# Performance work log

Measured on AMD Instinct MI355X. Metric: run time of the kernel, lower is better.

## Reference

```python
import jax, jax.numpy as jnp
import numpy as np

EPS = 1e-5

def setup_inputs() -> dict:
    key = jax.random.key(0)
    k1, k2 = jax.random.split(key)
    N, D, O = 32768, 4096, 256
    x = jax.random.normal(k1, (N, D), dtype=jnp.float32)
    gamma = jnp.ones((D,), dtype=jnp.float32)
    beta = jnp.zeros((D,), dtype=jnp.float32)
    W = jax.random.normal(k2, (O, D), dtype=jnp.float32) * (1.0 / np.sqrt(D))
    b = jnp.zeros((O,), dtype=jnp.float32)
    return {"x": x, "gamma": gamma, "beta": beta, "W": W, "b": b}


def reference(x, gamma, beta, W, b):
    # BatchNorm1d in training mode: per-feature batch mean and biased variance
    mean = jnp.mean(x, axis=0)                      # [D]
    var = jnp.mean(jnp.square(x - mean), axis=0)    # [D], biased (divide by N)
    xhat = (x - mean) * jax.lax.rsqrt(var + EPS)
    h = jax.nn.relu(xhat * gamma + beta)            # [N, D]
    # Linear projection
    return h @ W.T + b                               # [N, O]
```

## Files before the change

### kernel.cpp

```cpp
#include <hip/hip_runtime.h>
#include <hip/hip_bf16.h>

#define NROWS 32768
#define DDIM  4096
#define ODIM  256
#define EPSV  1e-5f

#define CHUNKS 128
#define RPC    256

#define BM 128
#define BK 64
#define NKT (DDIM / BK)

typedef __attribute__((ext_vector_type(4))) float          f32x4;
typedef __attribute__((ext_vector_type(8))) __bf16         bf16x8;
typedef __attribute__((ext_vector_type(8))) unsigned short u16x8;
typedef __attribute__((ext_vector_type(4))) unsigned short u16x4;

static __device__ __forceinline__ unsigned short f2bf(float f) {
  return __builtin_bit_cast(unsigned short, __float2bfloat16(f));
}

__global__ __launch_bounds__(256) void k1_stats(const float* __restrict__ x,
                                                float* __restrict__ psum,
                                                float* __restrict__ psq) {
  const int col = blockIdx.x * 1024 + threadIdx.x * 4;
  const float* p = x + (size_t)blockIdx.y * RPC * DDIM + col;
  f32x4 s = {0.f, 0.f, 0.f, 0.f};
  f32x4 q = {0.f, 0.f, 0.f, 0.f};
#pragma unroll 8
  for (int r = 0; r < RPC; ++r) {
    f32x4 v = *(const f32x4*)p;
    p += DDIM;
    s += v;
    q += v * v;
  }
  *(f32x4*)(psum + (size_t)blockIdx.y * DDIM + col) = s;
  *(f32x4*)(psq  + (size_t)blockIdx.y * DDIM + col) = q;
}

__global__ __launch_bounds__(256) void k2_stats_finalize(
    const float* __restrict__ psum, const float* __restrict__ psq,
    const float* __restrict__ gamma, const float* __restrict__ beta,
    float* __restrict__ scale, float* __restrict__ shift) {
  __shared__ float ss[4][64];
  __shared__ float sq[4][64];
  const int lane = threadIdx.x & 63;
  const int g    = threadIdx.x >> 6;
  const int d    = blockIdx.x * 64 + lane;
  float s = 0.f, qq = 0.f;
  for (int c = g * 32; c < (g + 1) * 32; ++c) {
    s  += psum[(size_t)c * DDIM + d];
    qq += psq [(size_t)c * DDIM + d];
  }
  ss[g][lane] = s;
  sq[g][lane] = qq;
  __syncthreads();
  if (g == 0) {
    s  = ss[0][lane] + ss[1][lane] + ss[2][lane] + ss[3][lane];
    qq = sq[0][lane] + sq[1][lane] + sq[2][lane] + sq[3][lane];
    const float inv = 1.0f / (float)NROWS;
    const float mean = s * inv;
    const float var  = fmaxf(qq * inv - mean * mean, 0.f);
    const float a = gamma[d] * rsqrtf(var + EPSV);
    scale[d] = a;
    shift[d] = beta[d] - mean * a;
  }
}

__global__ __launch_bounds__(256) void k2_wconv(const float* __restrict__ Wf,
                                                unsigned short* __restrict__ Wb) {
  const size_t i = ((size_t)blockIdx.x * 256 + threadIdx.x) * 4;
  f32x4 v = *(const f32x4*)(Wf + i);
  u16x4 o;
  o[0] = f2bf(v[0]); o[1] = f2bf(v[1]); o[2] = f2bf(v[2]); o[3] = f2bf(v[3]);
  *(u16x4*)(Wb + i) = o;
}

__global__ __launch_bounds__(512, 1) void k3_bn_gemm(
    const float* __restrict__ x,
    const unsigned short* __restrict__ Wb,
    const float* __restrict__ scale,
    const float* __restrict__ shift,
    const float* __restrict__ bias,
    float* __restrict__ out) {
  __shared__ unsigned short As[2][BM * BK];
  __shared__ unsigned short Bs[2][ODIM * BK];
  __shared__ float SF[DDIM];
  __shared__ float SH[DDIM];

  const int tid = threadIdx.x;
  const int l   = tid & 63;
  const int w   = tid >> 6;
  const int wr  = w >> 2;
  const int wc  = w & 3;
  const size_t bm0 = (size_t)blockIdx.x * BM;

  ((f32x4*)SF)[tid * 2]     = ((const f32x4*)scale)[tid * 2];
  ((f32x4*)SF)[tid * 2 + 1] = ((const f32x4*)scale)[tid * 2 + 1];
  ((f32x4*)SH)[tid * 2]     = ((const f32x4*)shift)[tid * 2];
  ((f32x4*)SH)[tid * 2 + 1] = ((const f32x4*)shift)[tid * 2 + 1];

  const int rA = tid >> 3;
  const int uA = tid & 7;
  const float* xp0 = x + (bm0 + rA) * (size_t)DDIM + uA * 8;
  const float* xp1 = xp0 + (size_t)64 * DDIM;
  const int awo = rA * 64 + ((uA ^ (rA & 7)) << 3);
  int ktb = uA * 8;

  const unsigned short* bsrc[4];
#pragma unroll
  for (int q = 0; q < 4; ++q) {
    const int p  = w * 256 + q * 64 + l;
    const int o  = p >> 3;
    const int up = p & 7;
    bsrc[q] = Wb + (size_t)o * DDIM + ((up ^ (o & 7)) << 3);
  }

  int offA[4], offB[4];
#pragma unroll
  for (int i = 0; i < 4; ++i) {
    const int row = wr * 64 + i * 16 + (l & 15);
    offA[i] = row * 64 + (((l >> 4) ^ (row & 7)) << 3);
  }
#pragma unroll
  for (int j = 0; j < 4; ++j) {
    const int row = wc * 64 + j * 16 + (l & 15);
    offB[j] = row * 64 + (((l >> 4) ^ (row & 7)) << 3);
  }

  const f32x4 zero = {0.f, 0.f, 0.f, 0.f};
  f32x4 acc[4][4];
#pragma unroll
  for (int i = 0; i < 4; ++i)
#pragma unroll
    for (int j = 0; j < 4; ++j) acc[i][j] = zero;

  f32x4 sA0[4], sA1[4];

#define ISSUE_A(S)                                                             \
  asm volatile("global_load_dwordx4 %0, %1, off" : "=v"(S[0]) : "v"(xp0));     \
  asm volatile("global_load_dwordx4 %0, %1, off" : "=v"(S[1]) : "v"(xp0 + 4)); \
  asm volatile("global_load_dwordx4 %0, %1, off" : "=v"(S[2]) : "v"(xp1));     \
  asm volatile("global_load_dwordx4 %0, %1, off" : "=v"(S[3]) : "v"(xp1 + 4)); \
  xp0 += BK; xp1 += BK;                                                        \
  asm volatile("" ::: "memory");

#define ISSUE_B(BUFI)                                                          \
  _Pragma("unroll")                                                            \
  for (int q = 0; q < 4; ++q) {                                                \
    __builtin_amdgcn_global_load_lds(                                          \
        (__attribute__((address_space(1))) void*)bsrc[q],                      \
        (__attribute__((address_space(3))) void*)(                             \
            &Bs[BUFI][(w * 256 + q * 64) * 8]),                                \
        16, 0, 0);                                                             \
    bsrc[q] += BK;                                                             \
  }                                                                            \
  asm volatile("" ::: "memory");

#define TRANSFORM_WRITE(BUFI, S)                                               \
  {                                                                            \
    f32x4 sa0 = *(const f32x4*)&SF[ktb];                                       \
    f32x4 sa1 = *(const f32x4*)&SF[ktb + 4];                                   \
    f32x4 sc0 = *(const f32x4*)&SH[ktb];                                       \
    f32x4 sc1 = *(const f32x4*)&SH[ktb + 4];                                   \
    ktb += BK;                                                                 \
    u16x8 pk0, pk1;                                                            \
    _Pragma("unroll")                                                          \
    for (int e = 0; e < 4; ++e) {                                              \
      pk0[e]     = f2bf(fmaxf(S[0][e] * sa0[e] + sc0[e], 0.f));                \
      pk0[e + 4] = f2bf(fmaxf(S[1][e] * sa1[e] + sc1[e], 0.f));                \
      pk1[e]     = f2bf(fmaxf(S[2][e] * sa0[e] + sc0[e], 0.f));                \
      pk1[e + 4] = f2bf(fmaxf(S[3][e] * sa1[e] + sc1[e], 0.f));                \
    }                                                                          \
    *(u16x8*)&As[BUFI][awo]        = pk0;                                      \
    *(u16x8*)&As[BUFI][awo + 4096] = pk1;                                      \
  }

#define MFMA_PHASE(BUFI)                                                       \
  _Pragma("unroll")                                                            \
  for (int kk = 0; kk < 2; ++kk) {                                             \
    const int kx = kk << 5;                                                    \
    bf16x8 af[4], bfr[4];                                                      \
    _Pragma("unroll")                                                          \
    for (int i = 0; i < 4; ++i)                                                \
      af[i] = __builtin_bit_cast(bf16x8,                                       \
                                 *(const u16x8*)&As[BUFI][offA[i] ^ kx]);      \
    _Pragma("unroll")                                                          \
    for (int j = 0; j < 4; ++j)                                                \
      bfr[j] = __builtin_bit_cast(bf16x8,                                      \
                                  *(const u16x8*)&Bs[BUFI][offB[j] ^ kx]);     \
    _Pragma("unroll")                                                          \
    for (int i = 0; i < 4; ++i)                                                \
      _Pragma("unroll")                                                        \
      for (int j = 0; j < 4; ++j)                                              \
        acc[i][j] = __builtin_amdgcn_mfma_f32_16x16x32_bf16(                   \
            af[i], bfr[j], acc[i][j], 0, 0, 0);                                \
  }

  {
    ISSUE_A(sA0);
    ISSUE_B(0);
    ISSUE_A(sA1);
    asm volatile("s_waitcnt lgkmcnt(0)" ::: "memory");
    __builtin_amdgcn_sched_barrier(0);
    __builtin_amdgcn_s_barrier();
    asm volatile("s_waitcnt vmcnt(8)" ::: "memory");
    __builtin_amdgcn_sched_barrier(0);
    TRANSFORM_WRITE(0, sA0);
    asm volatile("s_waitcnt vmcnt(4) lgkmcnt(0)" ::: "memory");
    __builtin_amdgcn_sched_barrier(0);
    __builtin_amdgcn_s_barrier();
  }

#define STEP_FULL(CUR, SC, SN)                                                 \
  do {                                                                         \
    ISSUE_B((CUR) ^ 1);                                                        \
    ISSUE_A(SC);                                                               \
    MFMA_PHASE(CUR);                                                           \
    asm volatile("s_waitcnt vmcnt(8)" ::: "memory");                           \
    __builtin_amdgcn_sched_barrier(0);                                         \
    TRANSFORM_WRITE((CUR) ^ 1, SN);                                            \
    asm volatile("s_waitcnt vmcnt(4) lgkmcnt(0)" ::: "memory");                \
    __builtin_amdgcn_sched_barrier(0);                                         \
    __builtin_amdgcn_s_barrier();                                              \
  } while (0)

  for (int kt = 0; kt < NKT - 2; kt += 2) {
    STEP_FULL(0, sA0, sA1);
    STEP_FULL(1, sA1, sA0);
  }
  {
    ISSUE_B(1);
    MFMA_PHASE(0);
    asm volatile("s_waitcnt vmcnt(4)" ::: "memory");
    __builtin_amdgcn_sched_barrier(0);
    TRANSFORM_WRITE(1, sA1);
    asm volatile("s_waitcnt vmcnt(0) lgkmcnt(0)" ::: "memory");
    __builtin_amdgcn_sched_barrier(0);
    __builtin_amdgcn_s_barrier();
  }
  MFMA_PHASE(1);

#undef STEP_FULL
#undef MFMA_PHASE
#undef TRANSFORM_WRITE
#undef ISSUE_B
#undef ISSUE_A

  const int cl = l & 15;
  const int rg = l >> 4;
#pragma unroll
  for (int j = 0; j < 4; ++j) {
    const int oc = wc * 64 + j * 16 + cl;
    const float bv = bias[oc];
#pragma unroll
    for (int i = 0; i < 4; ++i) {
      const size_t r0 = bm0 + wr * 64 + i * 16 + rg * 4;
#pragma unroll
      for (int rr = 0; rr < 4; ++rr) {
        out[(r0 + rr) * ODIM + oc] = acc[i][j][rr] + bv;
      }
    }
  }
}

extern "C" void kernel_launch(void* const* d_in, const int* in_sizes, int n_in,
                              void* d_out, int out_size, void* d_ws, size_t ws_size,
                              hipStream_t stream) {
  const float* x     = (const float*)d_in[0];
  const float* gamma = (const float*)d_in[1];
  const float* beta  = (const float*)d_in[2];
  const float* W     = (const float*)d_in[3];
  const float* b     = (const float*)d_in[4];
  float* out = (float*)d_out;

  float* psum  = (float*)d_ws;
  float* psq   = psum + (size_t)CHUNKS * DDIM;
  float* scale = psum + 2 * (size_t)CHUNKS * DDIM;
  float* shift = scale + DDIM;
  unsigned short* Wb = (unsigned short*)(shift + DDIM);

  k1_stats<<<dim3(4, CHUNKS), 256, 0, stream>>>(x, psum, psq);
  k2_stats_finalize<<<DDIM / 64, 256, 0, stream>>>(psum, psq, gamma, beta, scale, shift);
  k2_wconv<<<(ODIM * DDIM) / 1024, 256, 0, stream>>>(W, Wb);
  k3_bn_gemm<<<NROWS / BM, 512, 0, stream>>>(x, Wb, scale, shift, b, out);
}
```

Measured before the change: 246.7 us.

## Warp-specialize BN-GEMM into producer and MFMA consumer waves

Restructures the fused BN+GEMM kernel into 768-thread blocks in which 4 producer waves load x, apply the BN scale/shift/ReLU, convert to bf16 and fill the LDS buffers, while 8 consumer waves only run MFMAs on double-buffered tiles. The aim is to take global-load latency and transform work off the MFMA waves and overlap them through barrier-separated ping-pong stages. In exchange the producers carry twice the load and transform work per thread, and every stage now ends in a full block barrier. The launch bounds change to (768,3), which tightens the register budget.

```diff
diff --git a/kernel.cpp b/kernel.cpp
--- a/kernel.cpp
+++ b/kernel.cpp
@@ -78,7 +78,7 @@
   *(u16x4*)(Wb + i) = o;
 }
 
-__global__ __launch_bounds__(512, 1) void k3_bn_gemm(
+__global__ __launch_bounds__(768, 3) void k3_bn_gemm(
     const float* __restrict__ x,
     const unsigned short* __restrict__ Wb,
     const float* __restrict__ scale,
@@ -92,32 +92,12 @@
 
   const int tid = threadIdx.x;
   const int l   = tid & 63;
-  const int w   = tid >> 6;
-  const int wr  = w >> 2;
-  const int wc  = w & 3;
   const size_t bm0 = (size_t)blockIdx.x * BM;
-
-  ((f32x4*)SF)[tid * 2]     = ((const f32x4*)scale)[tid * 2];
-  ((f32x4*)SF)[tid * 2 + 1] = ((const f32x4*)scale)[tid * 2 + 1];
-  ((f32x4*)SH)[tid * 2]     = ((const f32x4*)shift)[tid * 2];
-  ((f32x4*)SH)[tid * 2 + 1] = ((const f32x4*)shift)[tid * 2 + 1];
-
-  const int rA = tid >> 3;
-  const int uA = tid & 7;
-  const float* xp0 = x + (bm0 + rA) * (size_t)DDIM + uA * 8;
-  const float* xp1 = xp0 + (size_t)64 * DDIM;
-  const int awo = rA * 64 + ((uA ^ (rA & 7)) << 3);
-  int ktb = uA * 8;
-
-  const unsigned short* bsrc[4];
-#pragma unroll
-  for (int q = 0; q < 4; ++q) {
-    const int p  = w * 256 + q * 64 + l;
-    const int o  = p >> 3;
-    const int up = p & 7;
-    bsrc[q] = Wb + (size_t)o * DDIM + ((up ^ (o & 7)) << 3);
-  }
-
+  const bool consumer = (tid < 512);
+
+  const int w  = tid >> 6;
+  const int wr = w >> 2;
+  const int wc = w & 3;
   int offA[4], offB[4];
 #pragma unroll
   for (int i = 0; i < 4; ++i) {
@@ -129,7 +109,6 @@
     const int row = wc * 64 + j * 16 + (l & 15);
     offB[j] = row * 64 + (((l >> 4) ^ (row & 7)) << 3);
   }
-
   const f32x4 zero = {0.f, 0.f, 0.f, 0.f};
   f32x4 acc[4][4];
 #pragma unroll
@@ -137,46 +116,89 @@
 #pragma unroll
     for (int j = 0; j < 4; ++j) acc[i][j] = zero;
 
-  f32x4 sA0[4], sA1[4];
-
-#define ISSUE_A(S)                                                             \
-  asm volatile("global_load_dwordx4 %0, %1, off" : "=v"(S[0]) : "v"(xp0));     \
-  asm volatile("global_load_dwordx4 %0, %1, off" : "=v"(S[1]) : "v"(xp0 + 4)); \
-  asm volatile("global_load_dwordx4 %0, %1, off" : "=v"(S[2]) : "v"(xp1));     \
-  asm volatile("global_load_dwordx4 %0, %1, off" : "=v"(S[3]) : "v"(xp1 + 4)); \
-  xp0 += BK; xp1 += BK;                                                        \
+  const int p  = tid - 512;
+  const int r0 = (p >> 3) & 31;
+  const int uA = p & 7;
+  const float* xr0 = x + (bm0 + r0) * (size_t)DDIM + uA * 8;
+  const float* xr1 = xr0 + (size_t)32 * DDIM;
+  const float* xr2 = xr0 + (size_t)64 * DDIM;
+  const float* xr3 = xr0 + (size_t)96 * DDIM;
+  const int awo = r0 * 64 + ((uA ^ (r0 & 7)) << 3);
+  int ktb = uA * 8;
+  const unsigned short* bsrc[8];
+#pragma unroll
+  for (int q = 0; q < 8; ++q) {
+    const int u  = q * 256 + p;
+    const int o  = u >> 3;
+    const int up = u & 7;
+    bsrc[q] = Wb + (size_t)o * DDIM + ((up ^ (o & 7)) << 3);
+  }
+  const int pwbase = (p & ~63);
+
+  if (!consumer) {
+    const int c0 = p * 16;
+#pragma unroll
+    for (int e = 0; e < 4; ++e) {
+      *(f32x4*)&SF[c0 + e * 4] = *(const f32x4*)(scale + c0 + e * 4);
+      *(f32x4*)&SH[c0 + e * 4] = *(const f32x4*)(shift + c0 + e * 4);
+    }
+  }
+  __syncthreads();
+
+#define ISSUE_A8(S)                                                            \
+  asm volatile("global_load_dwordx4 %0, %1, off"           : "=v"(S[0]) : "v"(xr0)); \
+  asm volatile("global_load_dwordx4 %0, %1, off offset:16" : "=v"(S[1]) : "v"(xr0)); \
+  asm volatile("global_load_dwordx4 %0, %1, off"           : "=v"(S[2]) : "v"(xr1)); \
+  asm volatile("global_load_dwordx4 %0, %1, off offset:16" : "=v"(S[3]) : "v"(xr1)); \
+  asm volatile("global_load_dwordx4 %0, %1, off"           : "=v"(S[4]) : "v"(xr2)); \
+  asm volatile("global_load_dwordx4 %0, %1, off offset:16" : "=v"(S[5]) : "v"(xr2)); \
+  asm volatile("global_load_dwordx4 %0, %1, off"           : "=v"(S[6]) : "v"(xr3)); \
+  asm volatile("global_load_dwordx4 %0, %1, off offset:16" : "=v"(S[7]) : "v"(xr3)); \
+  xr0 += BK; xr1 += BK; xr2 += BK; xr3 += BK;                                  \
   asm volatile("" ::: "memory");
 
-#define ISSUE_B(BUFI)                                                          \
+#define ISSUE_B8(BUFI)                                                         \
   _Pragma("unroll")                                                            \
-  for (int q = 0; q < 4; ++q) {                                                \
+  for (int q = 0; q < 8; ++q) {                                                \
     __builtin_amdgcn_global_load_lds(                                          \
         (__attribute__((address_space(1))) void*)bsrc[q],                      \
         (__attribute__((address_space(3))) void*)(                             \
-            &Bs[BUFI][(w * 256 + q * 64) * 8]),                                \
+            &Bs[BUFI][(q * 256 + pwbase) * 8]),                                \
         16, 0, 0);                                                             \
     bsrc[q] += BK;                                                             \
   }                                                                            \
   asm volatile("" ::: "memory");
 
-#define TRANSFORM_WRITE(BUFI, S)                                               \
+#define TRANSFORM4(BUFI, S)                                                    \
   {                                                                            \
     f32x4 sa0 = *(const f32x4*)&SF[ktb];                                       \
     f32x4 sa1 = *(const f32x4*)&SF[ktb + 4];                                   \
     f32x4 sc0 = *(const f32x4*)&SH[ktb];                                       \
     f32x4 sc1 = *(const f32x4*)&SH[ktb + 4];                                   \
     ktb += BK;                                                                 \
-    u16x8 pk0, pk1;                                                            \
-    _Pragma("unroll")                                                          \
-    for (int e = 0; e < 4; ++e) {                                              \
-      pk0[e]     = f2bf(fmaxf(S[0][e] * sa0[e] + sc0[e], 0.f));                \
-      pk0[e + 4] = f2bf(fmaxf(S[1][e] * sa1[e] + sc1[e], 0.f));                \
-      pk1[e]     = f2bf(fmaxf(S[2][e] * sa0[e] + sc0[e], 0.f));                \
-      pk1[e + 4] = f2bf(fmaxf(S[3][e] * sa1[e] + sc1[e], 0.f));                \
+    _Pragma("unroll")                                                          \
+    for (int k = 0; k < 4; ++k) {                                              \
+      u16x8 pk;                                                                \
+      _Pragma("unroll")                                                        \
+      for (int e = 0; e < 4; ++e) {                                            \
+        pk[e]     = f2bf(fmaxf(S[2 * k][e]     * sa0[e] + sc0[e], 0.f));       \
+        pk[e + 4] = f2bf(fmaxf(S[2 * k + 1][e] * sa1[e] + sc1[e], 0.f));       \
+      }                                                                        \
+      *(u16x8*)&As[BUFI][awo + k * 2048] = pk;                                 \
     }                                                                          \
-    *(u16x8*)&As[BUFI][awo]        = pk0;                                      \
-    *(u16x8*)&As[BUFI][awo + 4096] = pk1;                                      \
-  }
+  }
+
+#define PRODUCE(BUFI)                                                          \
+  do {                                                                         \
+    f32x4 S[8];                                                                \
+    ISSUE_A8(S);                                                               \
+    ISSUE_B8(BUFI);                                                            \
+    asm volatile("s_waitcnt vmcnt(8)" ::: "memory");                           \
+    __builtin_amdgcn_sched_barrier(0);                                         \
+    TRANSFORM4(BUFI, S);                                                       \
+    asm volatile("s_waitcnt vmcnt(0) lgkmcnt(0)" ::: "memory");                \
+    __builtin_amdgcn_sched_barrier(0);                                         \
+  } while (0)
 
 #define MFMA_PHASE(BUFI)                                                       \
   _Pragma("unroll")                                                            \
@@ -199,68 +221,39 @@
             af[i], bfr[j], acc[i][j], 0, 0, 0);                                \
   }
 
-  {
-    ISSUE_A(sA0);
-    ISSUE_B(0);
-    ISSUE_A(sA1);
-    asm volatile("s_waitcnt lgkmcnt(0)" ::: "memory");
-    __builtin_amdgcn_sched_barrier(0);
+  if (!consumer) PRODUCE(0);
+  __builtin_amdgcn_s_barrier();
+
+  for (int kt = 0; kt < NKT - 2; kt += 2) {
+    if (consumer) { MFMA_PHASE(0); } else { PRODUCE(1); }
     __builtin_amdgcn_s_barrier();
-    asm volatile("s_waitcnt vmcnt(8)" ::: "memory");
-    __builtin_amdgcn_sched_barrier(0);
-    TRANSFORM_WRITE(0, sA0);
-    asm volatile("s_waitcnt vmcnt(4) lgkmcnt(0)" ::: "memory");
-    __builtin_amdgcn_sched_barrier(0);
+    if (consumer) { MFMA_PHASE(1); } else { PRODUCE(0); }
     __builtin_amdgcn_s_barrier();
   }
-
-#define STEP_FULL(CUR, SC, SN)                                                 \
-  do {                                                                         \
-    ISSUE_B((CUR) ^ 1);                                                        \
-    ISSUE_A(SC);                                                               \
-    MFMA_PHASE(CUR);                                                           \
-    asm volatile("s_waitcnt vmcnt(8)" ::: "memory");                           \
-    __builtin_amdgcn_sched_barrier(0);                                         \
-    TRANSFORM_WRITE((CUR) ^ 1, SN);                                            \
-    asm volatile("s_waitcnt vmcnt(4) lgkmcnt(0)" ::: "memory");                \
-    __builtin_amdgcn_sched_barrier(0);                                         \
-    __builtin_amdgcn_s_barrier();                                              \
-  } while (0)
-
-  for (int kt = 0; kt < NKT - 2; kt += 2) {
-    STEP_FULL(0, sA0, sA1);
-    STEP_FULL(1, sA1, sA0);
-  }
-  {
-    ISSUE_B(1);
-    MFMA_PHASE(0);
-    asm volatile("s_waitcnt vmcnt(4)" ::: "memory");
-    __builtin_amdgcn_sched_barrier(0);
-    TRANSFORM_WRITE(1, sA1);
-    asm volatile("s_waitcnt vmcnt(0) lgkmcnt(0)" ::: "memory");
-    __builtin_amdgcn_sched_barrier(0);
-    __builtin_amdgcn_s_barrier();
-  }
-  MFMA_PHASE(1);
-
-#undef STEP_FULL
+  if (consumer) { MFMA_PHASE(0); } else { PRODUCE(1); }
+  __builtin_amdgcn_s_barrier();
+  if (consumer) { MFMA_PHASE(1); }
+
 #undef MFMA_PHASE
-#undef TRANSFORM_WRITE
-#undef ISSUE_B
-#undef ISSUE_A
-
-  const int cl = l & 15;
-  const int rg = l >> 4;
-#pragma unroll
-  for (int j = 0; j < 4; ++j) {
-    const int oc = wc * 64 + j * 16 + cl;
-    const float bv = bias[oc];
-#pragma unroll
-    for (int i = 0; i < 4; ++i) {
-      const size_t r0 = bm0 + wr * 64 + i * 16 + rg * 4;
-#pragma unroll
-      for (int rr = 0; rr < 4; ++rr) {
-        out[(r0 + rr) * ODIM + oc] = acc[i][j][rr] + bv;
+#undef PRODUCE
+#undef TRANSFORM4
+#undef ISSUE_B8
+#undef ISSUE_A8
+
+  if (consumer) {
+    const int cl = l & 15;
+    const int rg = l >> 4;
+#pragma unroll
+    for (int j = 0; j < 4; ++j) {
+      const int oc = wc * 64 + j * 16 + cl;
+      const float bv = bias[oc];
+#pragma unroll
+      for (int i = 0; i < 4; ++i) {
+        const size_t rbase = bm0 + wr * 64 + i * 16 + rg * 4;
+#pragma unroll
+        for (int rr = 0; rr < 4; ++rr) {
+          out[(rbase + rr) * ODIM + oc] = acc[i][j][rr] + bv;
+        }
       }
     }
   }
@@ -285,5 +278,5 @@
   k1_stats<<<dim3(4, CHUNKS), 256, 0, stream>>>(x, psum, psq);
   k2_stats_finalize<<<DDIM / 64, 256, 0, stream>>>(psum, psq, gamma, beta, scale, shift);
   k2_wconv<<<(ODIM * DDIM) / 1024, 256, 0, stream>>>(W, Wb);
-  k3_bn_gemm<<<NROWS / BM, 512, 0, stream>>>(x, Wb, scale, shift, b, out);
-}
+  k3_bn_gemm<<<NROWS / BM, 768, 0, stream>>>(x, Wb, scale, shift, b, out);
+}
```

Result: slower. 256.7 us (+4.1%).

## Feed A fragments straight from registers, dropping the LDS A tile

Applied to the files above, without the earlier changes.

Each wave now owns 16 full rows of the 128-row block and loads x directly in the layout the MFMA A operand expects. It normalizes and packs those values to bf16 in registers and passes them into the MFMA without staging through shared memory. Each wave computes all 256 output columns, so it reads 16 B fragments per k-step from LDS instead of 4 A plus 4 B. This removes the LDS writes and reads for A and the associated bank traffic. The cost is four times as many B-fragment LDS reads per wave and less reuse of each B load across rows.

```diff
diff --git a/kernel.cpp b/kernel.cpp
--- a/kernel.cpp
+++ b/kernel.cpp
@@ -85,7 +85,6 @@
     const float* __restrict__ shift,
     const float* __restrict__ bias,
     float* __restrict__ out) {
-  __shared__ unsigned short As[2][BM * BK];
   __shared__ unsigned short Bs[2][ODIM * BK];
   __shared__ float SF[DDIM];
   __shared__ float SH[DDIM];
@@ -93,21 +92,20 @@
   const int tid = threadIdx.x;
   const int l   = tid & 63;
   const int w   = tid >> 6;
-  const int wr  = w >> 2;
-  const int wc  = w & 3;
+  const int lr  = l & 15;
+  const int lc  = l >> 4;
   const size_t bm0 = (size_t)blockIdx.x * BM;
 
-  ((f32x4*)SF)[tid * 2]     = ((const f32x4*)scale)[tid * 2];
-  ((f32x4*)SF)[tid * 2 + 1] = ((const f32x4*)scale)[tid * 2 + 1];
-  ((f32x4*)SH)[tid * 2]     = ((const f32x4*)shift)[tid * 2];
-  ((f32x4*)SH)[tid * 2 + 1] = ((const f32x4*)shift)[tid * 2 + 1];
-
-  const int rA = tid >> 3;
-  const int uA = tid & 7;
-  const float* xp0 = x + (bm0 + rA) * (size_t)DDIM + uA * 8;
-  const float* xp1 = xp0 + (size_t)64 * DDIM;
-  const int awo = rA * 64 + ((uA ^ (rA & 7)) << 3);
-  int ktb = uA * 8;
+  {
+    const int c0 = tid * 8;
+    *(f32x4*)&SF[c0]     = *(const f32x4*)(scale + c0);
+    *(f32x4*)&SF[c0 + 4] = *(const f32x4*)(scale + c0 + 4);
+    *(f32x4*)&SH[c0]     = *(const f32x4*)(shift + c0);
+    *(f32x4*)&SH[c0 + 4] = *(const f32x4*)(shift + c0 + 4);
+  }
+
+  const float* xrp = x + (bm0 + w * 16 + lr) * (size_t)DDIM + lc * 8;
+  int ktb = 0;
 
   const unsigned short* bsrc[4];
 #pragma unroll
@@ -118,33 +116,22 @@
     bsrc[q] = Wb + (size_t)o * DDIM + ((up ^ (o & 7)) << 3);
   }
 
-  int offA[4], offB[4];
-#pragma unroll
-  for (int i = 0; i < 4; ++i) {
-    const int row = wr * 64 + i * 16 + (l & 15);
-    offA[i] = row * 64 + (((l >> 4) ^ (row & 7)) << 3);
-  }
-#pragma unroll
-  for (int j = 0; j < 4; ++j) {
-    const int row = wc * 64 + j * 16 + (l & 15);
-    offB[j] = row * 64 + (((l >> 4) ^ (row & 7)) << 3);
-  }
+  const int offB0 = lr * 64 + ((lc ^ (l & 7)) << 3);
 
   const f32x4 zero = {0.f, 0.f, 0.f, 0.f};
-  f32x4 acc[4][4];
-#pragma unroll
-  for (int i = 0; i < 4; ++i)
-#pragma unroll
-    for (int j = 0; j < 4; ++j) acc[i][j] = zero;
-
-  f32x4 sA0[4], sA1[4];
+  f32x4 acc[16];
+#pragma unroll
+  for (int j = 0; j < 16; ++j) acc[j] = zero;
+
+  f32x4 Ar0[4], Ar1[4];
+  u16x8 pk0a, pk0b, pk1a, pk1b;
 
 #define ISSUE_A(S)                                                             \
-  asm volatile("global_load_dwordx4 %0, %1, off" : "=v"(S[0]) : "v"(xp0));     \
-  asm volatile("global_load_dwordx4 %0, %1, off" : "=v"(S[1]) : "v"(xp0 + 4)); \
-  asm volatile("global_load_dwordx4 %0, %1, off" : "=v"(S[2]) : "v"(xp1));     \
-  asm volatile("global_load_dwordx4 %0, %1, off" : "=v"(S[3]) : "v"(xp1 + 4)); \
-  xp0 += BK; xp1 += BK;                                                        \
+  asm volatile("global_load_dwordx4 %0, %1, off"            : "=v"(S[0]) : "v"(xrp)); \
+  asm volatile("global_load_dwordx4 %0, %1, off offset:16"  : "=v"(S[1]) : "v"(xrp)); \
+  asm volatile("global_load_dwordx4 %0, %1, off offset:128" : "=v"(S[2]) : "v"(xrp)); \
+  asm volatile("global_load_dwordx4 %0, %1, off offset:144" : "=v"(S[3]) : "v"(xrp)); \
+  xrp += BK;                                                                   \
   asm volatile("" ::: "memory");
 
 #define ISSUE_B(BUFI)                                                          \
@@ -159,109 +146,96 @@
   }                                                                            \
   asm volatile("" ::: "memory");
 
-#define TRANSFORM_WRITE(BUFI, S)                                               \
+#define TRANSFORM(S, PKA, PKB)                                                 \
   {                                                                            \
-    f32x4 sa0 = *(const f32x4*)&SF[ktb];                                       \
-    f32x4 sa1 = *(const f32x4*)&SF[ktb + 4];                                   \
-    f32x4 sc0 = *(const f32x4*)&SH[ktb];                                       \
-    f32x4 sc1 = *(const f32x4*)&SH[ktb + 4];                                   \
+    const int tc = ktb + lc * 8;                                               \
+    f32x4 sa0 = *(const f32x4*)&SF[tc];                                        \
+    f32x4 sa1 = *(const f32x4*)&SF[tc + 4];                                    \
+    f32x4 ha0 = *(const f32x4*)&SH[tc];                                        \
+    f32x4 ha1 = *(const f32x4*)&SH[tc + 4];                                    \
+    f32x4 sb0 = *(const f32x4*)&SF[tc + 32];                                   \
+    f32x4 sb1 = *(const f32x4*)&SF[tc + 36];                                   \
+    f32x4 hb0 = *(const f32x4*)&SH[tc + 32];                                   \
+    f32x4 hb1 = *(const f32x4*)&SH[tc + 36];                                   \
     ktb += BK;                                                                 \
-    u16x8 pk0, pk1;                                                            \
     _Pragma("unroll")                                                          \
     for (int e = 0; e < 4; ++e) {                                              \
-      pk0[e]     = f2bf(fmaxf(S[0][e] * sa0[e] + sc0[e], 0.f));                \
-      pk0[e + 4] = f2bf(fmaxf(S[1][e] * sa1[e] + sc1[e], 0.f));                \
-      pk1[e]     = f2bf(fmaxf(S[2][e] * sa0[e] + sc0[e], 0.f));                \
-      pk1[e + 4] = f2bf(fmaxf(S[3][e] * sa1[e] + sc1[e], 0.f));                \
+      PKA[e]     = f2bf(fmaxf(S[0][e] * sa0[e] + ha0[e], 0.f));                \
+      PKA[e + 4] = f2bf(fmaxf(S[1][e] * sa1[e] + ha1[e], 0.f));                \
+      PKB[e]     = f2bf(fmaxf(S[2][e] * sb0[e] + hb0[e], 0.f));                \
+      PKB[e + 4] = f2bf(fmaxf(S[3][e] * sb1[e] + hb1[e], 0.f));                \
     }                                                                          \
-    *(u16x8*)&As[BUFI][awo]        = pk0;                                      \
-    *(u16x8*)&As[BUFI][awo + 4096] = pk1;                                      \
-  }
-
-#define MFMA_PHASE(BUFI)                                                       \
+  }
+
+#define MFMA_PHASE(CUR, PKA, PKB)                                              \
   _Pragma("unroll")                                                            \
   for (int kk = 0; kk < 2; ++kk) {                                             \
-    const int kx = kk << 5;                                                    \
-    bf16x8 af[4], bfr[4];                                                      \
+    const bf16x8 af = __builtin_bit_cast(bf16x8, kk ? PKB : PKA);              \
+    const int kbase = (offB0 ^ (kk << 5));                                     \
     _Pragma("unroll")                                                          \
-    for (int i = 0; i < 4; ++i)                                                \
-      af[i] = __builtin_bit_cast(bf16x8,                                       \
-                                 *(const u16x8*)&As[BUFI][offA[i] ^ kx]);      \
-    _Pragma("unroll")                                                          \
-    for (int j = 0; j < 4; ++j)                                                \
-      bfr[j] = __builtin_bit_cast(bf16x8,                                      \
-                                  *(const u16x8*)&Bs[BUFI][offB[j] ^ kx]);     \
-    _Pragma("unroll")                                                          \
-    for (int i = 0; i < 4; ++i)                                                \
-      _Pragma("unroll")                                                        \
-      for (int j = 0; j < 4; ++j)                                              \
-        acc[i][j] = __builtin_amdgcn_mfma_f32_16x16x32_bf16(                   \
-            af[i], bfr[j], acc[i][j], 0, 0, 0);                                \
+    for (int j = 0; j < 16; ++j) {                                             \
+      bf16x8 bf = __builtin_bit_cast(                                          \
+          bf16x8, *(const u16x8*)&Bs[CUR][kbase + j * 1024]);                  \
+      acc[j] = __builtin_amdgcn_mfma_f32_16x16x32_bf16(af, bf, acc[j], 0, 0, 0); \
+    }                                                                          \
   }
 
   {
-    ISSUE_A(sA0);
     ISSUE_B(0);
-    ISSUE_A(sA1);
+    ISSUE_A(Ar0);
+    ISSUE_A(Ar1);
     asm volatile("s_waitcnt lgkmcnt(0)" ::: "memory");
     __builtin_amdgcn_sched_barrier(0);
     __builtin_amdgcn_s_barrier();
-    asm volatile("s_waitcnt vmcnt(8)" ::: "memory");
-    __builtin_amdgcn_sched_barrier(0);
-    TRANSFORM_WRITE(0, sA0);
-    asm volatile("s_waitcnt vmcnt(4) lgkmcnt(0)" ::: "memory");
-    __builtin_amdgcn_sched_barrier(0);
+    asm volatile("s_waitcnt vmcnt(4)" ::: "memory");
+    __builtin_amdgcn_sched_barrier(0);
+    TRANSFORM(Ar0, pk0a, pk0b);
     __builtin_amdgcn_s_barrier();
   }
 
-#define STEP_FULL(CUR, SC, SN)                                                 \
+#define STEP(CUR, ARF, ART, PKCA, PKCB, PKNA, PKNB)                            \
   do {                                                                         \
     ISSUE_B((CUR) ^ 1);                                                        \
-    ISSUE_A(SC);                                                               \
-    MFMA_PHASE(CUR);                                                           \
-    asm volatile("s_waitcnt vmcnt(8)" ::: "memory");                           \
+    ISSUE_A(ARF);                                                              \
+    MFMA_PHASE(CUR, PKCA, PKCB);                                               \
+    asm volatile("s_waitcnt vmcnt(8)" ::: "memory");          \
     __builtin_amdgcn_sched_barrier(0);                                         \
-    TRANSFORM_WRITE((CUR) ^ 1, SN);                                            \
-    asm volatile("s_waitcnt vmcnt(4) lgkmcnt(0)" ::: "memory");                \
+    TRANSFORM(ART, PKNA, PKNB);                                                \
+    asm volatile("s_waitcnt vmcnt(4)" ::: "memory");        \
     __builtin_amdgcn_sched_barrier(0);                                         \
     __builtin_amdgcn_s_barrier();                                              \
   } while (0)
 
   for (int kt = 0; kt < NKT - 2; kt += 2) {
-    STEP_FULL(0, sA0, sA1);
-    STEP_FULL(1, sA1, sA0);
+    STEP(0, Ar0, Ar1, pk0a, pk0b, pk1a, pk1b);
+    STEP(1, Ar1, Ar0, pk1a, pk1b, pk0a, pk0b);
   }
   {
     ISSUE_B(1);
-    MFMA_PHASE(0);
+    MFMA_PHASE(0, pk0a, pk0b);
     asm volatile("s_waitcnt vmcnt(4)" ::: "memory");
     __builtin_amdgcn_sched_barrier(0);
-    TRANSFORM_WRITE(1, sA1);
+    TRANSFORM(Ar1, pk1a, pk1b);
     asm volatile("s_waitcnt vmcnt(0) lgkmcnt(0)" ::: "memory");
     __builtin_amdgcn_sched_barrier(0);
     __builtin_amdgcn_s_barrier();
   }
-  MFMA_PHASE(1);
-
-#undef STEP_FULL
+  MFMA_PHASE(1, pk1a, pk1b);
+
+#undef STEP
 #undef MFMA_PHASE
-#undef TRANSFORM_WRITE
+#undef TRANSFORM
 #undef ISSUE_B
 #undef ISSUE_A
 
-  const int cl = l & 15;
-  const int rg = l >> 4;
-#pragma unroll
-  for (int j = 0; j < 4; ++j) {
-    const int oc = wc * 64 + j * 16 + cl;
+#pragma unroll
+  for (int j = 0; j < 16; ++j) {
+    const int oc = j * 16 + lr;
     const float bv = bias[oc];
-#pragma unroll
-    for (int i = 0; i < 4; ++i) {
-      const size_t r0 = bm0 + wr * 64 + i * 16 + rg * 4;
-#pragma unroll
-      for (int rr = 0; rr < 4; ++rr) {
-        out[(r0 + rr) * ODIM + oc] = acc[i][j][rr] + bv;
-      }
+    const size_t r0 = bm0 + w * 16 + lc * 4;
+#pragma unroll
+    for (int rr = 0; rr < 4; ++rr) {
+      out[(r0 + rr) * ODIM + oc] = acc[j][rr] + bv;
     }
   }
 }
```

Measured after the change: 248.0 us. Within noise of the previous version (+0.5%).
